# Kernel tuning notes

Measured on AMD Instinct MI355X. Metric: run time of the kernel, lower is better.

Reference implementation:

```python
import jax, jax.numpy as jnp
import numpy as np

TEMPERATURE = 0.07
EPS = 1e-12  # matches torch F.normalize default eps


def setup_inputs() -> dict:
    key = jax.random.key(0)
    k1, k2 = jax.random.split(key)
    features1 = jax.random.normal(k1, (16384, 512), dtype=jnp.float32)
    features2 = jax.random.normal(k2, (16384, 512), dtype=jnp.float32)
    return {"features1": features1, "features2": features2}


def _l2_normalize(x):
    # torch F.normalize: x / max(||x||, eps)
    norm = jnp.sqrt(jnp.sum(x * x, axis=1, keepdims=True))
    return x / jnp.maximum(norm, EPS)


def reference(features1, features2):
    f1 = _l2_normalize(features1)
    f2 = _l2_normalize(features2)
    # [N, N] similarity logits
    logits = jnp.einsum('nd,md->nm', f1, f2) / TEMPERATURE
    n = logits.shape[0]
    # cross-entropy with labels = arange(n): mean over rows of (logsumexp - diag logit)
    log_probs = jax.nn.log_softmax(logits, axis=1)
    diag = jnp.diagonal(log_probs)
    loss = -jnp.mean(diag)
    return loss
```

## Files before the change

### kernel.cpp

```cpp
#include <hip/hip_runtime.h>
#include <stdint.h>

#define NROWS 16384
#define KDIM  512
#define BM 128
#define BN 256
#define CT 2
#define NCHUNK 32
#define NPH 16
#define SLOT 24576
#define INV_T 14.285714285714286f
#define LOG2E 1.4426950408889634f
#define LN2   0.6931471805599453f

typedef __bf16 bf16x8 __attribute__((ext_vector_type(8)));
typedef float  f32x16 __attribute__((ext_vector_type(16)));
typedef unsigned short u16x8 __attribute__((ext_vector_type(8)));

__device__ __forceinline__ void gload_lds16(const void* gptr, void* lptr) {
    uint32_t loff = (uint32_t)(uintptr_t)lptr;
    loff = __builtin_amdgcn_readfirstlane(loff);
    __builtin_amdgcn_global_load_lds(
        (const uint32_t __attribute__((address_space(1)))*)(uintptr_t)gptr,
        (uint32_t __attribute__((address_space(3)))*)(uintptr_t)loff,
        16, 0, 0);
}


__global__ void k_norm(const float* __restrict__ X, char* __restrict__ Y, float scale) {
    const int row  = blockIdx.x * 4 + (threadIdx.x >> 6);
    const int lane = threadIdx.x & 63;
    const float* xr = X + (size_t)row * KDIM + lane * 8;
    float4 a = *(const float4*)xr;
    float4 b = *(const float4*)(xr + 4);
    float ss = a.x*a.x + a.y*a.y + a.z*a.z + a.w*a.w
             + b.x*b.x + b.y*b.y + b.z*b.z + b.w*b.w;
    #pragma unroll
    for (int off = 1; off < 64; off <<= 1) ss += __shfl_xor(ss, off);
    const float s = scale / fmaxf(sqrtf(ss), 1e-12f);
    __bf16 o[8];
    o[0] = (__bf16)(a.x * s); o[1] = (__bf16)(a.y * s);
    o[2] = (__bf16)(a.z * s); o[3] = (__bf16)(a.w * s);
    o[4] = (__bf16)(b.x * s); o[5] = (__bf16)(b.y * s);
    o[6] = (__bf16)(b.z * s); o[7] = (__bf16)(b.w * s);
    const int kh = lane >> 2, q = lane & 3;
    const size_t gr = ((size_t)(kh * 512 + (row >> 5)) * 2 + (q >> 1)) * 64
                    + ((q & 1) << 5) + (row & 31);
    *(u16x8*)(Y + gr * 16) = *(const u16x8*)o;
}

__global__ __launch_bounds__(256, 2) void k_gemm(const char* __restrict__ A,
                                                 const char* __restrict__ B,
                                                 float* __restrict__ S_part) {
    __shared__ __align__(16) char L[3 * SLOT];
    __shared__ float rowsum[2][BM];
    char* Lc = (char*)L;

    const int tid  = threadIdx.x;
    const int lane = tid & 63;
    const int w    = tid >> 6;
    const int wr   = w >> 1, wc = w & 1;
    const int bid  = blockIdx.x;
    const int xcd  = bid & 7;
    const int idx  = bid >> 3;
    const int st   = idx >> 5;
    const int wsub = idx & 31;
    const int sg   = xcd * 16 + st;
    const int bg   = sg & 15, cg = sg >> 4;
    const int brow  = (bg * 8 + (wsub >> 2)) * BM;
    const int chunk = cg * 4 + (wsub & 3);
    const int rbA0 = brow >> 5;

#define STGA(KH_, S_) do {                                                    \
        const char* g_ = A + ((size_t)((KH_) * 512 + rbA0) * 2048) + tid * 16;\
        char* l_ = Lc + (S_) * SLOT + tid * 16;                               \
        gload_lds16(g_,        l_);                                           \
        gload_lds16(g_ + 4096, l_ + 4096);                                    \
    } while (0)

#define STGB(KH_, S_) do {                                                    \
        const char* g_ = B + ((size_t)((KH_) * 512 + rbB0) * 2048) + tid * 16;\
        char* l_ = Lc + (S_) * SLOT + 8192 + tid * 16;                        \
        gload_lds16(g_,         l_);                                          \
        gload_lds16(g_ +  4096, l_ +  4096);                                  \
        gload_lds16(g_ +  8192, l_ +  8192);                                  \
        gload_lds16(g_ + 12288, l_ + 12288);                                  \
    } while (0)

#define RDS(HH_) do {                                                         \
        const char* sl_ = Lc + ((HH_) % 3) * SLOT;                            \
        _Pragma("unroll") for (int m_ = 0; m_ < 2; ++m_)                      \
        _Pragma("unroll") for (int ks_ = 0; ks_ < 2; ++ks_)                   \
            af[m_][ks_] = *(const bf16x8*)(sl_ + ((wr * 2 + m_) << 11)        \
                                           + (ks_ << 10) + (lane << 4));      \
        _Pragma("unroll") for (int n_ = 0; n_ < 4; ++n_)                      \
        _Pragma("unroll") for (int ks_ = 0; ks_ < 2; ++ks_)                   \
            bf[n_][ks_] = *(const bf16x8*)(sl_ + 8192                         \
                  + ((wc * 4 + n_) << 11) + (ks_ << 10) + (lane << 4));       \
    } while (0)

#define MM() do {                                                             \
        __builtin_amdgcn_s_setprio(1);                                        \
        _Pragma("unroll") for (int m_ = 0; m_ < 2; ++m_)                      \
        _Pragma("unroll") for (int n_ = 0; n_ < 4; ++n_)                      \
        _Pragma("unroll") for (int ks_ = 0; ks_ < 2; ++ks_)                   \
            acc[m_][n_] = __builtin_amdgcn_mfma_f32_32x32x16_bf16(            \
                af[m_][ks_], bf[n_][ks_], acc[m_][n_], 0, 0, 0);              \
        __builtin_amdgcn_s_setprio(0);                                        \
    } while (0)

    float rowacc = 0.f;
    #pragma unroll 1
    for (int ct = 0; ct < CT; ++ct) {
        const int rbB0 = chunk * 16 + ct * 8;
        f32x16 acc[2][4] = {};
        bf16x8 af[2][2], bf[4][2];

        STGA(0, 0); STGB(0, 0);
        STGA(1, 1); STGB(1, 1);
        asm volatile("s_waitcnt vmcnt(6)" ::: "memory");
        __builtin_amdgcn_s_barrier();

        #pragma unroll
        for (int h = 0; h < NPH; ++h) {
            RDS(h);
            if (h < NPH - 2) { STGA(h + 2, (h + 2) % 3); STGB(h + 2, (h + 2) % 3); }
            MM();
            if (h < NPH - 2)       asm volatile("s_waitcnt vmcnt(6)" ::: "memory");
            else if (h == NPH - 2) asm volatile("s_waitcnt vmcnt(0)" ::: "memory");
            __builtin_amdgcn_s_barrier();
        }

        #pragma unroll
        for (int m = 0; m < 2; ++m) {
            float rs[16];
            #pragma unroll
            for (int r = 0; r < 16; ++r)
                rs[r] = __builtin_amdgcn_exp2f(acc[m][0][r])
                      + __builtin_amdgcn_exp2f(acc[m][1][r])
                      + __builtin_amdgcn_exp2f(acc[m][2][r])
                      + __builtin_amdgcn_exp2f(acc[m][3][r]);
            #pragma unroll
            for (int off = 16; off >= 1; off >>= 1)
                #pragma unroll
                for (int r = 0; r < 16; ++r)
                    rs[r] += __shfl_xor(rs[r], off);
            if ((lane & 31) == 0) {
                const int rb = wr * 64 + m * 32 + (lane >> 5) * 4;
                #pragma unroll
                for (int r = 0; r < 16; ++r)
                    rowsum[wc][rb + (r & 3) + 8 * (r >> 2)] = rs[r];
            }
        }
        __syncthreads();
        if (tid < BM) rowacc += rowsum[0][tid] + rowsum[1][tid];
        __syncthreads();
    }
#undef STGA
#undef STGB
#undef RDS
#undef MM
    if (tid < BM) S_part[(size_t)chunk * NROWS + brow + tid] = rowacc;
}

__global__ void k_diag(const char* __restrict__ A, const char* __restrict__ B,
                       float* __restrict__ diag) {
    const int row  = blockIdx.x * 4 + (threadIdx.x >> 6);
    const int lane = threadIdx.x & 63;
    const int kh = lane >> 2, q = lane & 3;
    const size_t gr = ((size_t)(kh * 512 + (row >> 5)) * 2 + (q >> 1)) * 64
                    + ((q & 1) << 5) + (row & 31);
    const bf16x8 va = *(const bf16x8*)(A + gr * 16);
    const bf16x8 vb = *(const bf16x8*)(B + gr * 16);
    float d = 0.f;
    #pragma unroll
    for (int i = 0; i < 8; ++i) d += (float)va[i] * (float)vb[i];
    #pragma unroll
    for (int off2 = 1; off2 < 64; off2 <<= 1) d += __shfl_xor(d, off2);
    if (lane == 0) diag[row] = d;
}

__global__ void k_loss(const float* __restrict__ S_part, const float* __restrict__ diag,
                       float* __restrict__ partial) {
    const int g = blockIdx.x * 256 + threadIdx.x;
    float S = 0.f;
    #pragma unroll
    for (int c = 0; c < NCHUNK; ++c) S += S_part[(size_t)c * NROWS + g];
    float v = logf(S) - diag[g] * LN2;
    __shared__ float wsum[4];
    #pragma unroll
    for (int off = 1; off < 64; off <<= 1) v += __shfl_xor(v, off);
    if ((threadIdx.x & 63) == 0) wsum[threadIdx.x >> 6] = v;
    __syncthreads();
    if (threadIdx.x == 0) partial[blockIdx.x] = wsum[0] + wsum[1] + wsum[2] + wsum[3];
}

__global__ void k_final(const float* __restrict__ partial, float* __restrict__ out) {
    float v = partial[threadIdx.x];
    #pragma unroll
    for (int off = 1; off < 64; off <<= 1) v += __shfl_xor(v, off);
    if (threadIdx.x == 0) out[0] = v * (1.0f / (float)NROWS);
}

extern "C" void kernel_launch(void* const* d_in, const int* in_sizes, int n_in,
                              void* d_out, int out_size, void* d_ws, size_t ws_size,
                              hipStream_t stream) {
    const float* f1 = (const float*)d_in[0];
    const float* f2 = (const float*)d_in[1];
    float* out = (float*)d_out;

    char* ws = (char*)d_ws;
    char*  f1p   = ws;
    char*  f2p   = ws + (16u << 20);
    float* S_part = (float*)(ws + (32u << 20));
    float* diag   = (float*)(ws + (34u << 20));
    float* part   = (float*)(ws + (34u << 20) + (1u << 16));

    k_norm<<<dim3(NROWS / 4), dim3(256), 0, stream>>>(f1, f1p, INV_T * LOG2E);
    k_norm<<<dim3(NROWS / 4), dim3(256), 0, stream>>>(f2, f2p, 1.0f);
    k_gemm<<<dim3((NROWS / BM) * NCHUNK), dim3(256), 0, stream>>>(f1p, f2p, S_part);
    k_diag<<<dim3(NROWS / 4), dim3(256), 0, stream>>>(f1p, f2p, diag);
    k_loss<<<dim3(NROWS / 256), dim3(256), 0, stream>>>(S_part, diag, part);
    k_final<<<dim3(1), dim3(64), 0, stream>>>(part, out);
}
```

Before: 350.2 us.

## Shrink GEMM N-tile to 128 and compute diagonal in fp32 from raw inputs

Halves the GEMM block's N tile from 256 to 128 and doubles the column-tile loop count. This cuts LDS per stage, the B-tile loads and the accumulator registers, which may raise occupancy but lowers A-tile reuse per load. The diagonal logit is now computed in fp32 from the original inputs, with norms computed inline, instead of from the bf16 packed copies. This makes the diagonal more accurate but adds a read of the full fp32 inputs.

```diff
diff --git a/kernel.cpp b/kernel.cpp
--- a/kernel.cpp
+++ b/kernel.cpp
@@ -4,14 +4,13 @@
 #define NROWS 16384
 #define KDIM  512
 #define BM 128
-#define BN 256
-#define CT 2
+#define BN 128
+#define CT 4
 #define NCHUNK 32
 #define NPH 16
-#define SLOT 24576
+#define SLOT 16384
 #define INV_T 14.285714285714286f
 #define LOG2E 1.4426950408889634f
-#define LN2   0.6931471805599453f
 
 typedef __bf16 bf16x8 __attribute__((ext_vector_type(8)));
 typedef float  f32x16 __attribute__((ext_vector_type(16)));
@@ -81,10 +80,8 @@
 #define STGB(KH_, S_) do {                                                    \
         const char* g_ = B + ((size_t)((KH_) * 512 + rbB0) * 2048) + tid * 16;\
         char* l_ = Lc + (S_) * SLOT + 8192 + tid * 16;                        \
-        gload_lds16(g_,         l_);                                          \
-        gload_lds16(g_ +  4096, l_ +  4096);                                  \
-        gload_lds16(g_ +  8192, l_ +  8192);                                  \
-        gload_lds16(g_ + 12288, l_ + 12288);                                  \
+        gload_lds16(g_,        l_);                                           \
+        gload_lds16(g_ + 4096, l_ + 4096);                                    \
     } while (0)
 
 #define RDS(HH_) do {                                                         \
@@ -93,16 +90,16 @@
         _Pragma("unroll") for (int ks_ = 0; ks_ < 2; ++ks_)                   \
             af[m_][ks_] = *(const bf16x8*)(sl_ + ((wr * 2 + m_) << 11)        \
                                            + (ks_ << 10) + (lane << 4));      \
-        _Pragma("unroll") for (int n_ = 0; n_ < 4; ++n_)                      \
+        _Pragma("unroll") for (int n_ = 0; n_ < 2; ++n_)                      \
         _Pragma("unroll") for (int ks_ = 0; ks_ < 2; ++ks_)                   \
-            bf[n_][ks_] = *(const bf16x8*)(sl_ + 8192                         \
-                  + ((wc * 4 + n_) << 11) + (ks_ << 10) + (lane << 4));       \
+            bf[n_][ks_] = *(const bf16x8*)(sl_ + 8192 + ((wc * 2 + n_) << 11) \
+                                           + (ks_ << 10) + (lane << 4));      \
     } while (0)
 
 #define MM() do {                                                             \
         __builtin_amdgcn_s_setprio(1);                                        \
         _Pragma("unroll") for (int m_ = 0; m_ < 2; ++m_)                      \
-        _Pragma("unroll") for (int n_ = 0; n_ < 4; ++n_)                      \
+        _Pragma("unroll") for (int n_ = 0; n_ < 2; ++n_)                      \
         _Pragma("unroll") for (int ks_ = 0; ks_ < 2; ++ks_)                   \
             acc[m_][n_] = __builtin_amdgcn_mfma_f32_32x32x16_bf16(            \
                 af[m_][ks_], bf[n_][ks_], acc[m_][n_], 0, 0, 0);              \
@@ -112,13 +109,13 @@
     float rowacc = 0.f;
     #pragma unroll 1
     for (int ct = 0; ct < CT; ++ct) {
-        const int rbB0 = chunk * 16 + ct * 8;
-        f32x16 acc[2][4] = {};
-        bf16x8 af[2][2], bf[4][2];
+        const int rbB0 = chunk * 16 + ct * 4;
+        f32x16 acc[2][2] = {};
+        bf16x8 af[2][2], bf[2][2];
 
         STGA(0, 0); STGB(0, 0);
         STGA(1, 1); STGB(1, 1);
-        asm volatile("s_waitcnt vmcnt(6)" ::: "memory");
+        asm volatile("s_waitcnt vmcnt(4)" ::: "memory");
         __builtin_amdgcn_s_barrier();
 
         #pragma unroll
@@ -126,7 +123,7 @@
             RDS(h);
             if (h < NPH - 2) { STGA(h + 2, (h + 2) % 3); STGB(h + 2, (h + 2) % 3); }
             MM();
-            if (h < NPH - 2)       asm volatile("s_waitcnt vmcnt(6)" ::: "memory");
+            if (h < NPH - 2)       asm volatile("s_waitcnt vmcnt(4)" ::: "memory");
             else if (h == NPH - 2) asm volatile("s_waitcnt vmcnt(0)" ::: "memory");
             __builtin_amdgcn_s_barrier();
         }
@@ -137,9 +134,7 @@
             #pragma unroll
             for (int r = 0; r < 16; ++r)
                 rs[r] = __builtin_amdgcn_exp2f(acc[m][0][r])
-                      + __builtin_amdgcn_exp2f(acc[m][1][r])
-                      + __builtin_amdgcn_exp2f(acc[m][2][r])
-                      + __builtin_amdgcn_exp2f(acc[m][3][r]);
+                      + __builtin_amdgcn_exp2f(acc[m][1][r]);
             #pragma unroll
             for (int off = 16; off >= 1; off >>= 1)
                 #pragma unroll
@@ -163,21 +158,28 @@
     if (tid < BM) S_part[(size_t)chunk * NROWS + brow + tid] = rowacc;
 }
 
-__global__ void k_diag(const char* __restrict__ A, const char* __restrict__ B,
+__global__ void k_diag(const float* __restrict__ X1, const float* __restrict__ X2,
                        float* __restrict__ diag) {
     const int row  = blockIdx.x * 4 + (threadIdx.x >> 6);
     const int lane = threadIdx.x & 63;
-    const int kh = lane >> 2, q = lane & 3;
-    const size_t gr = ((size_t)(kh * 512 + (row >> 5)) * 2 + (q >> 1)) * 64
-                    + ((q & 1) << 5) + (row & 31);
-    const bf16x8 va = *(const bf16x8*)(A + gr * 16);
-    const bf16x8 vb = *(const bf16x8*)(B + gr * 16);
-    float d = 0.f;
-    #pragma unroll
-    for (int i = 0; i < 8; ++i) d += (float)va[i] * (float)vb[i];
-    #pragma unroll
-    for (int off2 = 1; off2 < 64; off2 <<= 1) d += __shfl_xor(d, off2);
-    if (lane == 0) diag[row] = d;
+    const float* x1 = X1 + (size_t)row * KDIM + lane * 8;
+    const float* x2 = X2 + (size_t)row * KDIM + lane * 8;
+    float4 a0 = *(const float4*)x1, a1 = *(const float4*)(x1 + 4);
+    float4 b0 = *(const float4*)x2, b1 = *(const float4*)(x2 + 4);
+    float s1 = a0.x*a0.x + a0.y*a0.y + a0.z*a0.z + a0.w*a0.w
+             + a1.x*a1.x + a1.y*a1.y + a1.z*a1.z + a1.w*a1.w;
+    float s2 = b0.x*b0.x + b0.y*b0.y + b0.z*b0.z + b0.w*b0.w
+             + b1.x*b1.x + b1.y*b1.y + b1.z*b1.z + b1.w*b1.w;
+    float dd = a0.x*b0.x + a0.y*b0.y + a0.z*b0.z + a0.w*b0.w
+             + a1.x*b1.x + a1.y*b1.y + a1.z*b1.z + a1.w*b1.w;
+    #pragma unroll
+    for (int off = 1; off < 64; off <<= 1) {
+        s1 += __shfl_xor(s1, off);
+        s2 += __shfl_xor(s2, off);
+        dd += __shfl_xor(dd, off);
+    }
+    if (lane == 0)
+        diag[row] = dd / (fmaxf(sqrtf(s1), 1e-12f) * fmaxf(sqrtf(s2), 1e-12f)) * INV_T;
 }
 
 __global__ void k_loss(const float* __restrict__ S_part, const float* __restrict__ diag,
@@ -186,7 +188,7 @@
     float S = 0.f;
     #pragma unroll
     for (int c = 0; c < NCHUNK; ++c) S += S_part[(size_t)c * NROWS + g];
-    float v = logf(S) - diag[g] * LN2;
+    float v = logf(S) - diag[g];
     __shared__ float wsum[4];
     #pragma unroll
     for (int off = 1; off < 64; off <<= 1) v += __shfl_xor(v, off);
@@ -219,7 +221,7 @@
     k_norm<<<dim3(NROWS / 4), dim3(256), 0, stream>>>(f1, f1p, INV_T * LOG2E);
     k_norm<<<dim3(NROWS / 4), dim3(256), 0, stream>>>(f2, f2p, 1.0f);
     k_gemm<<<dim3((NROWS / BM) * NCHUNK), dim3(256), 0, stream>>>(f1p, f2p, S_part);
-    k_diag<<<dim3(NROWS / 4), dim3(256), 0, stream>>>(f1p, f2p, diag);
+    k_diag<<<dim3(NROWS / 4), dim3(256), 0, stream>>>(f1, f2, diag);
     k_loss<<<dim3(NROWS / 256), dim3(256), 0, stream>>>(S_part, diag, part);
     k_final<<<dim3(1), dim3(64), 0, stream>>>(part, out);
 }
```

Result: no change. 354.4 us (+1.2%).
